# Kernel tuning notes

Measured on AMD Instinct MI355X. Metric: run time of the kernel, lower is better.

The kernel has to match this reference:

```python
import jax, jax.numpy as jnp
import numpy as np

B, T, C = 128, 512, 512
EPS = 1e-5


def setup_inputs() -> dict:
    key = jax.random.key(0)
    ks = jax.random.split(key, 12)
    s_tri = 1.0 / np.sqrt(T)   # rough torch Linear init scale (per-row fan-in varies; fixed for simplicity)
    s_fc1 = 1.0 / np.sqrt(C)
    s_fc2 = 1.0 / np.sqrt(2 * C)
    return {
        "inputs": jax.random.normal(ks[0], (B, T, C), dtype=jnp.float32),
        "ln1_w": jnp.ones((T, C), jnp.float32),
        "ln1_b": jnp.zeros((T, C), jnp.float32),
        "ln2_w": jnp.ones((T, C), jnp.float32),
        "ln2_b": jnp.zeros((T, C), jnp.float32),
        # Row s of triu_W corresponds to nn.Linear(s+1, 1); entries j> s are masked in reference().
        "triu_W": jax.random.uniform(ks[1], (T, T), jnp.float32, -s_tri, s_tri),
        "triu_b": jax.random.uniform(ks[2], (T,), jnp.float32, -s_tri, s_tri),
        "fc1_W": jax.random.uniform(ks[3], (2 * C, C), jnp.float32, -s_fc1, s_fc1),
        "fc1_b": jax.random.uniform(ks[4], (2 * C,), jnp.float32, -s_fc1, s_fc1),
        "fc2_W": jax.random.uniform(ks[5], (C, 2 * C), jnp.float32, -s_fc2, s_fc2),
        "fc2_b": jax.random.uniform(ks[6], (C,), jnp.float32, -s_fc2, s_fc2),
    }


def _layernorm_2d(x, w, b):
    # torch nn.LayerNorm((T, C)): normalize jointly over the last TWO dims.
    mu = jnp.mean(x, axis=(-2, -1), keepdims=True)
    var = jnp.var(x, axis=(-2, -1), keepdims=True)
    return (x - mu) * jax.lax.rsqrt(var + EPS) * w + b


def reference(inputs, ln1_w, ln1_b, ln2_w, ln2_b, triu_W, triu_b, fc1_W, fc1_b, fc2_W, fc2_b):
    x = _layernorm_2d(inputs, ln1_w, ln1_b)                       # [B,T,C]
    # TriU time mixer on x.mT ([B,C,T]): out[..., s] = sum_{t<=s} W[s,t]*x[..., t] + b[s]
    Wm = jnp.tril(triu_W)                                          # causal mask
    xm = jnp.einsum('btc,st->bsc', x, Wm) + triu_b[None, :, None]  # [B,T,C] (already back-transposed)
    x2 = _layernorm_2d(xm + inputs, ln2_w, ln2_b)                  # [B,T,C]
    h = jax.nn.gelu(jnp.einsum('btc,hc->bth', x2, fc1_W) + fc1_b, approximate=False)
    y = jnp.einsum('bth,ch->btc', h, fc2_W) + fc2_b
    return x2 + y
```

## Files before the change

### kernel.cpp

```cpp
#include <hip/hip_runtime.h>
#include <cstdint>

typedef unsigned short u16;
typedef __attribute__((ext_vector_type(8))) short s16x8;
typedef __attribute__((ext_vector_type(4))) float f32x4;
typedef __attribute__((ext_vector_type(8))) unsigned short u16x8;
typedef __attribute__((ext_vector_type(4))) unsigned short u16x4;

#define B_ 128
#define T_ 512
#define C_ 512
#define TC 262144

static __device__ __forceinline__ float bf2f(u16 u) {
  union { unsigned int i; float f; } v; v.i = ((unsigned int)u) << 16; return v.f;
}
static __device__ __forceinline__ u16 f2bf(float f) {
  union { float fv; unsigned int i; } v; v.fv = f;
  unsigned int r = (v.i + 0x7FFFu + ((v.i >> 16) & 1u)) >> 16;
  return (u16)r;
}

static __device__ __forceinline__ float gelu_fast(float x) {
  float x2 = x * x;
  float arg = 1.5957691216057308f * x * fmaf(0.044715f, x2, 1.0f);
  return x / (1.0f + __expf(-arg));
}

#define GLD16(gp, lp) __builtin_amdgcn_global_load_lds( \
    (const __attribute__((address_space(1))) void*)(gp), \
    (__attribute__((address_space(3))) void*)(lp), 16, 0, 0)


__global__ __launch_bounds__(256)
void reduce_stats_kernel(const float* __restrict__ X, float2* __restrict__ partials) {
  const int b = blockIdx.y, blk = blockIdx.x, tid = threadIdx.x;
  const float* p = X + (size_t)b * TC + (size_t)blk * 2048 + (size_t)tid * 8;
  f32x4 v0 = *(const f32x4*)p;
  f32x4 v1 = *(const f32x4*)(p + 4);
  float s = 0.f, q = 0.f;
#pragma unroll
  for (int i = 0; i < 4; ++i) { s += v0[i] + v1[i]; q += v0[i] * v0[i] + v1[i] * v1[i]; }
  for (int o = 32; o; o >>= 1) { s += __shfl_down(s, o); q += __shfl_down(q, o); }
  __shared__ float ss[4], qq[4];
  if ((tid & 63) == 0) { ss[tid >> 6] = s; qq[tid >> 6] = q; }
  __syncthreads();
  if (tid == 0)
    partials[(size_t)b * 128 + blk] =
        make_float2(ss[0] + ss[1] + ss[2] + ss[3], qq[0] + qq[1] + qq[2] + qq[3]);
}

__global__ __launch_bounds__(128)
void finalize_stats_kernel(const float2* __restrict__ partials, float2* __restrict__ stats) {
  const int b = blockIdx.x, tid = threadIdx.x;
  float2 v = partials[(size_t)b * 128 + tid];
  float s = v.x, q = v.y;
  for (int o = 32; o; o >>= 1) { s += __shfl_down(s, o); q += __shfl_down(q, o); }
  __shared__ float ss[2], qq[2];
  if ((tid & 63) == 0) { ss[tid >> 6] = s; qq[tid >> 6] = q; }
  __syncthreads();
  if (tid == 0) {
    float sm = ss[0] + ss[1], sq = qq[0] + qq[1];
    float mean = sm * (1.f / (float)TC);
    float var = sq * (1.f / (float)TC) - mean * mean;
    stats[b] = make_float2(mean, rsqrtf(var + 1e-5f));
  }
}

__global__ __launch_bounds__(64)
void finalize_stats4_kernel(const float2* __restrict__ partials, float2* __restrict__ stats) {
  const int b = blockIdx.x, tid = threadIdx.x;
  float s = 0.f, q = 0.f;
  if (tid < 4) { float2 v = partials[(size_t)b * 4 + tid]; s = v.x; q = v.y; }
  for (int o = 2; o; o >>= 1) { s += __shfl_down(s, o); q += __shfl_down(q, o); }
  if (tid == 0) {
    float mean = s * (1.f / (float)TC);
    float var = q * (1.f / (float)TC) - mean * mean;
    stats[b] = make_float2(mean, rsqrtf(var + 1e-5f));
  }
}


__global__ __launch_bounds__(256)
void ln1_transpose_kernel(const float* __restrict__ X, const float* __restrict__ W,
                          const float* __restrict__ Bv, const float2* __restrict__ stats,
                          u16* __restrict__ xT) {
  const int b = blockIdx.z;
  const int t0 = blockIdx.y * 64, c0 = blockIdx.x * 64;
  const float2 st = stats[b];
  const float mu = st.x, rs = st.y;
  __shared__ u16 tile[64][72];
  const int tid = threadIdx.x;
  const int rr = tid >> 4;
  const int cc = (tid & 15) * 4;
#pragma unroll
  for (int i = 0; i < 4; ++i) {
    const int lt = i * 16 + rr;
    const size_t wi = (size_t)(t0 + lt) * C_ + c0 + cc;
    f32x4 x = *(const f32x4*)(X + (size_t)b * TC + wi);
    f32x4 w = *(const f32x4*)(W + wi);
    f32x4 bb = *(const f32x4*)(Bv + wi);
#pragma unroll
    for (int j = 0; j < 4; ++j)
      tile[lt][cc + j] = f2bf((x[j] - mu) * rs * w[j] + bb[j]);
  }
  __syncthreads();
  const int c = tid >> 2;
  const int tg = (tid & 3) * 16;
  u16 buf[16];
#pragma unroll
  for (int i = 0; i < 16; ++i) buf[i] = tile[tg + i][c];
  const size_t o = (size_t)b * TC + (size_t)(c0 + c) * T_ + t0 + tg;
  u16x8 o0, o1;
#pragma unroll
  for (int i = 0; i < 8; ++i) { o0[i] = buf[i]; o1[i] = buf[8 + i]; }
  *(u16x8*)(xT + o) = o0;
  *(u16x8*)(xT + o + 8) = o1;
}


__global__ __launch_bounds__(256)
void ln2_apply_kernel(const u16* __restrict__ S, const float* __restrict__ W,
                      const float* __restrict__ Bv, const float2* __restrict__ stats,
                      u16* __restrict__ x2) {
  const size_t i = ((size_t)blockIdx.x * 256 + threadIdx.x) * 8;
  const int b = (int)(i >> 18);
  const size_t r = i & (size_t)(TC - 1);
  const float2 st = stats[b];
  const float mu = st.x, rs = st.y;
  u16x8 sv = *(const u16x8*)(S + i);
  f32x4 w0 = *(const f32x4*)(W + r);
  f32x4 w1 = *(const f32x4*)(W + r + 4);
  f32x4 b0 = *(const f32x4*)(Bv + r);
  f32x4 b1 = *(const f32x4*)(Bv + r + 4);
  u16x8 o;
#pragma unroll
  for (int j = 0; j < 4; ++j) {
    o[j]     = f2bf((bf2f(sv[j])     - mu) * rs * w0[j] + b0[j]);
    o[4 + j] = f2bf((bf2f(sv[4 + j]) - mu) * rs * w1[j] + b1[j]);
  }
  *(u16x8*)(x2 + i) = o;
}


__global__ __launch_bounds__(256)
void cvt_bf16_kernel(const float* __restrict__ X, u16* __restrict__ Y) {
  const size_t i = ((size_t)blockIdx.x * 256 + threadIdx.x) * 4;
  f32x4 v = *(const f32x4*)(X + i);
  u16x4 o;
#pragma unroll
  for (int j = 0; j < 4; ++j) o[j] = f2bf(v[j]);
  *(u16x4*)(Y + i) = o;
}

__global__ __launch_bounds__(256)
void tril_bf16_kernel(const float* __restrict__ Wt, u16* __restrict__ Y) {
  const int i = blockIdx.x * 256 + threadIdx.x;
  const int s = i >> 9, t = i & 511;
  Y[i] = f2bf(t <= s ? Wt[i] : 0.f);
}


template <int MODE>
__global__ __launch_bounds__(512, 1)
void gemm_bt_kernel(const u16* __restrict__ A, const u16* __restrict__ Bm,
                    int K, int lda, int ldb,
                    void* __restrict__ Cp, int ldc,
                    const float* __restrict__ bias,
                    const void* __restrict__ res,
                    long long strideB, long long strideC,
                    float2* __restrict__ stat_part) {
  __shared__ u16 Asb[2 * 16384];
  __shared__ u16 Bsb[2 * 16384];
  __shared__ float rs_[8], rq_[8];
  const int tid = threadIdx.x;

  const int nwg = gridDim.x;
  const int orig = blockIdx.x;
  const int swz = (orig & 7) * (nwg >> 3) + (orig >> 3);
  int bx, by, bz;
  if (MODE == 0) { bz = swz >> 2; by = (swz >> 1) & 1; bx = swz & 1; }
  else if (MODE == 1) { bz = 0; by = swz >> 2; bx = swz & 3; }
  else { bz = 0; by = swz >> 1; bx = swz & 1; }

  const u16* Bp = Bm + (size_t)bz * (size_t)strideB;
  const int m0 = by * 256, n0 = bx * 256;
  int kTiles = K >> 6;
  if (MODE == 0) { const int need = (by + 1) * 4; if (need < kTiles) kTiles = need; }

  const int lane = tid & 63;
  const int wave = tid >> 6;
  const int wm = (wave >> 2) * 128;
  const int wn = (wave & 3) * 64;
  const int lr = lane & 15;
  const int kg = lane >> 4;

  f32x4 acc[8][4];
  const f32x4 zero = {0.f, 0.f, 0.f, 0.f};
#pragma unroll
  for (int m = 0; m < 8; ++m)
#pragma unroll
    for (int n = 0; n < 4; ++n) acc[m][n] = zero;

  auto STAGE_A = [&](int t) {
    const int k0 = t << 6;
    const int d = (t & 1) * 16384;
#pragma unroll
    for (int p = 0; p < 4; ++p) {
      const int q = p * 512 + tid;
      const int r = q >> 3;
      const int kcs = (q & 7) ^ (r & 7);
      GLD16(A + (size_t)(m0 + r) * lda + k0 + (kcs << 3), &Asb[d + q * 8]);
    }
  };
  auto STAGE_B = [&](int t) {
    const int k0 = t << 6;
    const int d = (t & 1) * 16384;
#pragma unroll
    for (int p = 0; p < 4; ++p) {
      const int q = p * 512 + tid;
      const int r = q >> 3;
      const int kcs = (q & 7) ^ (r & 7);
      GLD16(Bp + (size_t)(n0 + r) * ldb + k0 + (kcs << 3), &Bsb[d + q * 8]);
    }
  };

  STAGE_A(0); STAGE_B(0); STAGE_A(1);

  for (int kt = 0; kt < kTiles; ++kt) {
    const int d = (kt & 1) * 16384;

    if (kt + 1 < kTiles) asm volatile("s_waitcnt vmcnt(4)" ::: "memory");
    else                 asm volatile("s_waitcnt vmcnt(0)" ::: "memory");
    __builtin_amdgcn_s_barrier();
    asm volatile("" ::: "memory");

    s16x8 a0[8], a1[8], b0[4], b1[4];
#pragma unroll
    for (int m = 0; m < 8; ++m) {
      const int row = wm + m * 16 + lr;
      const u16* base = &Asb[d + row * 64];
      a0[m] = *(const s16x8*)(base + (((kg)     ^ (row & 7)) << 3));
      a1[m] = *(const s16x8*)(base + (((4 + kg) ^ (row & 7)) << 3));
    }
#pragma unroll
    for (int n = 0; n < 4; ++n) {
      const int row = wn + n * 16 + lr;
      b0[n] = *(const s16x8*)(&Bsb[d + row * 64] + (((kg) ^ (row & 7)) << 3));
    }
    if (kt + 1 < kTiles) STAGE_B(kt + 1);

    __builtin_amdgcn_s_setprio(1);
#pragma unroll
    for (int m = 0; m < 8; ++m)
#pragma unroll
      for (int n = 0; n < 4; ++n)
        acc[m][n] = __builtin_amdgcn_mfma_f32_16x16x32_bf16(a0[m], b0[n], acc[m][n], 0, 0, 0);
    __builtin_amdgcn_s_setprio(0);

#pragma unroll
    for (int n = 0; n < 4; ++n) {
      const int row = wn + n * 16 + lr;
      b1[n] = *(const s16x8*)(&Bsb[d + row * 64] + (((4 + kg) ^ (row & 7)) << 3));
    }
    asm volatile("s_waitcnt lgkmcnt(0)" ::: "memory");
    __builtin_amdgcn_s_barrier();
    asm volatile("" ::: "memory");
    if (kt + 2 < kTiles) STAGE_A(kt + 2);

    __builtin_amdgcn_s_setprio(1);
#pragma unroll
    for (int m = 0; m < 8; ++m)
#pragma unroll
      for (int n = 0; n < 4; ++n)
        acc[m][n] = __builtin_amdgcn_mfma_f32_16x16x32_bf16(a1[m], b1[n], acc[m][n], 0, 0, 0);
    __builtin_amdgcn_s_setprio(0);
  }

  if (MODE == 0) {
    u16* Cptr = (u16*)Cp + (size_t)bz * (size_t)strideC;
    const float* inp = (const float*)res + (size_t)bz * (size_t)strideC;
    float psum = 0.f, psq = 0.f;
#pragma unroll
    for (int m = 0; m < 8; ++m) {
      const int rb = m0 + wm + m * 16 + kg * 4;
#pragma unroll
      for (int n = 0; n < 4; ++n) {
        const int col = n0 + wn + n * 16 + lr;
#pragma unroll
        for (int j = 0; j < 4; ++j) {
          const size_t idx = (size_t)(rb + j) * ldc + col;
          float v = acc[m][n][j] + inp[idx] + bias[rb + j];
          psum += v; psq += v * v;
          Cptr[idx] = f2bf(v);
        }
      }
    }
    for (int o = 32; o; o >>= 1) { psum += __shfl_down(psum, o); psq += __shfl_down(psq, o); }
    if (lane == 0) { rs_[wave] = psum; rq_[wave] = psq; }
    __syncthreads();
    if (tid == 0) {
      float s = 0.f, q = 0.f;
#pragma unroll
      for (int w = 0; w < 8; ++w) { s += rs_[w]; q += rq_[w]; }
      stat_part[(size_t)bz * 4 + by * 2 + bx] = make_float2(s, q);
    }
  } else if (MODE == 1) {
    u16* Cptr = (u16*)Cp;
#pragma unroll
    for (int m = 0; m < 8; ++m) {
      const int rb = m0 + wm + m * 16 + kg * 4;
#pragma unroll
      for (int n = 0; n < 4; ++n) {
        const int col = n0 + wn + n * 16 + lr;
        const float bs = bias[col];
#pragma unroll
        for (int j = 0; j < 4; ++j) {
          float v = acc[m][n][j] + bs;
          Cptr[(size_t)(rb + j) * ldc + col] = f2bf(gelu_fast(v));
        }
      }
    }
  } else {
    float* Cptr = (float*)Cp;
    const u16* x2p = (const u16*)res;
#pragma unroll
    for (int m = 0; m < 8; ++m) {
      const int rb = m0 + wm + m * 16 + kg * 4;
#pragma unroll
      for (int n = 0; n < 4; ++n) {
        const int col = n0 + wn + n * 16 + lr;
        const float bs = bias[col];
#pragma unroll
        for (int j = 0; j < 4; ++j) {
          const size_t idx = (size_t)(rb + j) * ldc + col;
          Cptr[idx] = acc[m][n][j] + bs + bf2f(x2p[idx]);
        }
      }
    }
  }
}


extern "C" void kernel_launch(void* const* d_in, const int* in_sizes, int n_in,
                              void* d_out, int out_size, void* d_ws, size_t ws_size,
                              hipStream_t stream) {
  const float* inputs = (const float*)d_in[0];
  const float* ln1_w  = (const float*)d_in[1];
  const float* ln1_b  = (const float*)d_in[2];
  const float* ln2_w  = (const float*)d_in[3];
  const float* ln2_b  = (const float*)d_in[4];
  const float* triu_W = (const float*)d_in[5];
  const float* triu_b = (const float*)d_in[6];
  const float* fc1_W  = (const float*)d_in[7];
  const float* fc1_b  = (const float*)d_in[8];
  const float* fc2_W  = (const float*)d_in[9];
  const float* fc2_b  = (const float*)d_in[10];
  float* out = (float*)d_out;
  (void)in_sizes; (void)n_in; (void)out_size; (void)ws_size;

  char* ws = (char*)d_ws;
  size_t off = 0;
  auto carve = [&](size_t bytes) {
    char* p = ws + off;
    off += (bytes + 255) & ~(size_t)255;
    return p;
  };
  u16* s_bf = (u16*)carve((size_t)B_ * T_ * C_ * 2);
  u16* xT   = (u16*)carve((size_t)B_ * T_ * C_ * 2);
  u16* x2   = xT;
  u16* h    = (u16*)carve((size_t)B_ * T_ * 2 * C_ * 2);
  u16* wmb  = (u16*)carve((size_t)T_ * T_ * 2);
  u16* w1b  = (u16*)carve((size_t)2 * C_ * C_ * 2);
  u16* w2b  = (u16*)carve((size_t)C_ * 2 * C_ * 2);
  float2* partials  = (float2*)carve(128 * 128 * sizeof(float2));
  float2* partials2 = (float2*)carve(128 * 4 * sizeof(float2));
  float2* stats1 = (float2*)carve(128 * sizeof(float2));
  float2* stats2 = (float2*)carve(128 * sizeof(float2));

  reduce_stats_kernel<<<dim3(128, 128), 256, 0, stream>>>(inputs, partials);
  finalize_stats_kernel<<<128, 128, 0, stream>>>(partials, stats1);
  ln1_transpose_kernel<<<dim3(8, 8, 128), 256, 0, stream>>>(inputs, ln1_w, ln1_b, stats1, xT);
  tril_bf16_kernel<<<1024, 256, 0, stream>>>(triu_W, wmb);
  cvt_bf16_kernel<<<512, 256, 0, stream>>>(fc1_W, w1b);
  cvt_bf16_kernel<<<512, 256, 0, stream>>>(fc2_W, w2b);
  gemm_bt_kernel<0><<<512, 512, 0, stream>>>(
      wmb, xT, 512, 512, 512, s_bf, 512, triu_b, inputs, (long long)TC, (long long)TC, partials2);
  finalize_stats4_kernel<<<128, 64, 0, stream>>>(partials2, stats2);
  ln2_apply_kernel<<<16384, 256, 0, stream>>>(s_bf, ln2_w, ln2_b, stats2, x2);
  gemm_bt_kernel<1><<<1024, 512, 0, stream>>>(
      x2, w1b, 512, 512, 512, h, 1024, fc1_b, nullptr, 0, 0, nullptr);
  gemm_bt_kernel<2><<<512, 512, 0, stream>>>(
      h, w2b, 1024, 1024, 1024, out, 512, fc2_b, x2, 0, 0, nullptr);
}
```

Measured before the change: 373.3 us.

## Load GEMM weights directly from global into registers, triple-buffer activations

For the FC GEMM modes, the weight (B) operand is no longer staged through shared memory; each wave loads its B fragments straight from global memory into registers, and the A tile gets a third LDS buffer so two tiles can be in flight ahead. This drops B LDS writes and reads and one barrier per k-step, and frees LDS for the extra A stage. The cost is uncached-by-LDS global loads of weights that are duplicated across waves, and the register loads may stall the MFMA issue if L2 latency isn't hidden. The vmcnt(4) wait count also now has the register loads mixed into the counter, which could make the synchronisation fragile.

```diff
diff --git a/kernel.cpp b/kernel.cpp
--- a/kernel.cpp
+++ b/kernel.cpp
@@ -170,8 +170,9 @@
                     const void* __restrict__ res,
                     long long strideB, long long strideC,
                     float2* __restrict__ stat_part) {
-  __shared__ u16 Asb[2 * 16384];
-  __shared__ u16 Bsb[2 * 16384];
+  constexpr int ABUFS = (MODE == 0) ? 2 : 3;
+  __shared__ u16 Asb[ABUFS * 16384];
+  __shared__ u16 Bsb[(MODE == 0) ? 2 * 16384 : 16];
   __shared__ float rs_[8], rq_[8];
   const int tid = threadIdx.x;
 
@@ -202,9 +203,9 @@
 #pragma unroll
     for (int n = 0; n < 4; ++n) acc[m][n] = zero;
 
-  auto STAGE_A = [&](int t) {
+  auto STAGE_A = [&](int t, int buf) {
     const int k0 = t << 6;
-    const int d = (t & 1) * 16384;
+    const int d = buf * 16384;
 #pragma unroll
     for (int p = 0; p < 4; ++p) {
       const int q = p * 512 + tid;
@@ -225,56 +226,101 @@
     }
   };
 
-  STAGE_A(0); STAGE_B(0); STAGE_A(1);
-
-  for (int kt = 0; kt < kTiles; ++kt) {
-    const int d = (kt & 1) * 16384;
-
-    if (kt + 1 < kTiles) asm volatile("s_waitcnt vmcnt(4)" ::: "memory");
-    else                 asm volatile("s_waitcnt vmcnt(0)" ::: "memory");
-    __builtin_amdgcn_s_barrier();
-    asm volatile("" ::: "memory");
-
-    s16x8 a0[8], a1[8], b0[4], b1[4];
-#pragma unroll
-    for (int m = 0; m < 8; ++m) {
-      const int row = wm + m * 16 + lr;
-      const u16* base = &Asb[d + row * 64];
-      a0[m] = *(const s16x8*)(base + (((kg)     ^ (row & 7)) << 3));
-      a1[m] = *(const s16x8*)(base + (((4 + kg) ^ (row & 7)) << 3));
-    }
-#pragma unroll
-    for (int n = 0; n < 4; ++n) {
-      const int row = wn + n * 16 + lr;
-      b0[n] = *(const s16x8*)(&Bsb[d + row * 64] + (((kg) ^ (row & 7)) << 3));
-    }
-    if (kt + 1 < kTiles) STAGE_B(kt + 1);
-
-    __builtin_amdgcn_s_setprio(1);
-#pragma unroll
-    for (int m = 0; m < 8; ++m)
-#pragma unroll
-      for (int n = 0; n < 4; ++n)
-        acc[m][n] = __builtin_amdgcn_mfma_f32_16x16x32_bf16(a0[m], b0[n], acc[m][n], 0, 0, 0);
-    __builtin_amdgcn_s_setprio(0);
-
-#pragma unroll
-    for (int n = 0; n < 4; ++n) {
-      const int row = wn + n * 16 + lr;
-      b1[n] = *(const s16x8*)(&Bsb[d + row * 64] + (((4 + kg) ^ (row & 7)) << 3));
-    }
-    asm volatile("s_waitcnt lgkmcnt(0)" ::: "memory");
-    __builtin_amdgcn_s_barrier();
-    asm volatile("" ::: "memory");
-    if (kt + 2 < kTiles) STAGE_A(kt + 2);
-
-    __builtin_amdgcn_s_setprio(1);
-#pragma unroll
-    for (int m = 0; m < 8; ++m)
-#pragma unroll
-      for (int n = 0; n < 4; ++n)
-        acc[m][n] = __builtin_amdgcn_mfma_f32_16x16x32_bf16(a1[m], b1[n], acc[m][n], 0, 0, 0);
-    __builtin_amdgcn_s_setprio(0);
+  if (MODE == 0) {
+    STAGE_A(0, 0); STAGE_B(0); STAGE_A(1, 1);
+    for (int kt = 0; kt < kTiles; ++kt) {
+      const int d = (kt & 1) * 16384;
+      if (kt + 1 < kTiles) asm volatile("s_waitcnt vmcnt(4)" ::: "memory");
+      else                 asm volatile("s_waitcnt vmcnt(0)" ::: "memory");
+      __builtin_amdgcn_s_barrier();
+      asm volatile("" ::: "memory");
+
+      s16x8 a0[8], a1[8], b0[4], b1[4];
+#pragma unroll
+      for (int m = 0; m < 8; ++m) {
+        const int row = wm + m * 16 + lr;
+        const u16* base = &Asb[d + row * 64];
+        a0[m] = *(const s16x8*)(base + (((kg)     ^ (row & 7)) << 3));
+        a1[m] = *(const s16x8*)(base + (((4 + kg) ^ (row & 7)) << 3));
+      }
+#pragma unroll
+      for (int n = 0; n < 4; ++n) {
+        const int row = wn + n * 16 + lr;
+        b0[n] = *(const s16x8*)(&Bsb[d + row * 64] + (((kg) ^ (row & 7)) << 3));
+      }
+      if (kt + 1 < kTiles) STAGE_B(kt + 1);
+
+      __builtin_amdgcn_s_setprio(1);
+#pragma unroll
+      for (int m = 0; m < 8; ++m)
+#pragma unroll
+        for (int n = 0; n < 4; ++n)
+          acc[m][n] = __builtin_amdgcn_mfma_f32_16x16x32_bf16(a0[m], b0[n], acc[m][n], 0, 0, 0);
+      __builtin_amdgcn_s_setprio(0);
+
+#pragma unroll
+      for (int n = 0; n < 4; ++n) {
+        const int row = wn + n * 16 + lr;
+        b1[n] = *(const s16x8*)(&Bsb[d + row * 64] + (((4 + kg) ^ (row & 7)) << 3));
+      }
+      asm volatile("s_waitcnt lgkmcnt(0)" ::: "memory");
+      __builtin_amdgcn_s_barrier();
+      asm volatile("" ::: "memory");
+      if (kt + 2 < kTiles) STAGE_A(kt + 2, kt & 1);
+
+      __builtin_amdgcn_s_setprio(1);
+#pragma unroll
+      for (int m = 0; m < 8; ++m)
+#pragma unroll
+        for (int n = 0; n < 4; ++n)
+          acc[m][n] = __builtin_amdgcn_mfma_f32_16x16x32_bf16(a1[m], b1[n], acc[m][n], 0, 0, 0);
+      __builtin_amdgcn_s_setprio(0);
+    }
+  } else {
+    int rb0 = 0, rb1 = 1, rb2 = 2;
+    STAGE_A(0, 0); STAGE_A(1, 1);
+    for (int kt = 0; kt < kTiles; ++kt) {
+      const int k0 = kt << 6;
+      if (kt + 1 < kTiles) asm volatile("s_waitcnt vmcnt(4)" ::: "memory");
+      else                 asm volatile("s_waitcnt vmcnt(0)" ::: "memory");
+      __builtin_amdgcn_s_barrier();
+      asm volatile("" ::: "memory");
+
+      s16x8 w0[4], w1[4];
+#pragma unroll
+      for (int n = 0; n < 4; ++n) {
+        const u16* wrow = Bp + (size_t)(n0 + wn + n * 16 + lr) * ldb + k0 + (kg << 3);
+        w0[n] = *(const s16x8*)wrow;
+        w1[n] = *(const s16x8*)(wrow + 32);
+      }
+      asm volatile("" ::: "memory");
+      if (kt + 2 < kTiles) STAGE_A(kt + 2, rb2);
+
+      const int d = rb0 * 16384;
+      s16x8 a0[8], a1[8];
+#pragma unroll
+      for (int m = 0; m < 8; ++m) {
+        const int row = wm + m * 16 + lr;
+        const u16* base = &Asb[d + row * 64];
+        a0[m] = *(const s16x8*)(base + (((kg)     ^ (row & 7)) << 3));
+        a1[m] = *(const s16x8*)(base + (((4 + kg) ^ (row & 7)) << 3));
+      }
+
+      __builtin_amdgcn_s_setprio(1);
+#pragma unroll
+      for (int m = 0; m < 8; ++m)
+#pragma unroll
+        for (int n = 0; n < 4; ++n)
+          acc[m][n] = __builtin_amdgcn_mfma_f32_16x16x32_bf16(a0[m], w0[n], acc[m][n], 0, 0, 0);
+#pragma unroll
+      for (int m = 0; m < 8; ++m)
+#pragma unroll
+        for (int n = 0; n < 4; ++n)
+          acc[m][n] = __builtin_amdgcn_mfma_f32_16x16x32_bf16(a1[m], w1[n], acc[m][n], 0, 0, 0);
+      __builtin_amdgcn_s_setprio(0);
+
+      const int t = rb0; rb0 = rb1; rb1 = rb2; rb2 = t;
+    }
   }
 
   if (MODE == 0) {
```

After: 457.9 us. +22.7%, slower.

## Use FP8 for FC2 GEMM and bf16 copy of inputs for LN1 and residual

Applied to the files above, without the earlier changes.

The GELU output h and the fc2 weights are now stored as FP8 e4m3, and the FC2 GEMM runs on fp8 MFMA with half-size LDS tiles, allowing two blocks per CU. The stats reduction also writes a bf16 copy of the inputs, which the LN1 transpose and the triu GEMM residual read instead of fp32. This halves memory traffic for h and the input re-reads and doubles MFMA throughput for FC2. In exchange it loses precision, since FP8 h with GELU outputs and the bf16 residual may push the error past tolerance, and it adds an extra write of the inputs.

```diff
diff --git a/kernel.cpp b/kernel.cpp
--- a/kernel.cpp
+++ b/kernel.cpp
@@ -1,11 +1,14 @@
 #include <hip/hip_runtime.h>
+#include <hip/hip_fp8.h>
 #include <cstdint>
 
 typedef unsigned short u16;
+typedef unsigned char u8;
 typedef __attribute__((ext_vector_type(8))) short s16x8;
 typedef __attribute__((ext_vector_type(4))) float f32x4;
 typedef __attribute__((ext_vector_type(8))) unsigned short u16x8;
 typedef __attribute__((ext_vector_type(4))) unsigned short u16x4;
+typedef __attribute__((ext_vector_type(4))) unsigned char u8x4;
 
 #define B_ 128
 #define T_ 512
@@ -20,6 +23,10 @@
   unsigned int r = (v.i + 0x7FFFu + ((v.i >> 16) & 1u)) >> 16;
   return (u16)r;
 }
+static __device__ __forceinline__ u8 f2fp8(float f) {
+  __hip_fp8_e4m3 v(f);
+  return *(u8*)&v;
+}
 
 static __device__ __forceinline__ float gelu_fast(float x) {
   float x2 = x * x;
@@ -33,14 +40,21 @@
 
 
 __global__ __launch_bounds__(256)
-void reduce_stats_kernel(const float* __restrict__ X, float2* __restrict__ partials) {
+void reduce_stats_kernel(const float* __restrict__ X, float2* __restrict__ partials,
+                         u16* __restrict__ Xb) {
   const int b = blockIdx.y, blk = blockIdx.x, tid = threadIdx.x;
-  const float* p = X + (size_t)b * TC + (size_t)blk * 2048 + (size_t)tid * 8;
+  const size_t gi = (size_t)b * TC + (size_t)blk * 2048 + (size_t)tid * 8;
+  const float* p = X + gi;
   f32x4 v0 = *(const f32x4*)p;
   f32x4 v1 = *(const f32x4*)(p + 4);
   float s = 0.f, q = 0.f;
-#pragma unroll
-  for (int i = 0; i < 4; ++i) { s += v0[i] + v1[i]; q += v0[i] * v0[i] + v1[i] * v1[i]; }
+  u16x8 ob;
+#pragma unroll
+  for (int i = 0; i < 4; ++i) {
+    s += v0[i] + v1[i]; q += v0[i] * v0[i] + v1[i] * v1[i];
+    ob[i] = f2bf(v0[i]); ob[4 + i] = f2bf(v1[i]);
+  }
+  *(u16x8*)(Xb + gi) = ob;
   for (int o = 32; o; o >>= 1) { s += __shfl_down(s, o); q += __shfl_down(q, o); }
   __shared__ float ss[4], qq[4];
   if ((tid & 63) == 0) { ss[tid >> 6] = s; qq[tid >> 6] = q; }
@@ -82,7 +96,7 @@
 
 
 __global__ __launch_bounds__(256)
-void ln1_transpose_kernel(const float* __restrict__ X, const float* __restrict__ W,
+void ln1_transpose_kernel(const u16* __restrict__ Xb, const float* __restrict__ W,
                           const float* __restrict__ Bv, const float2* __restrict__ stats,
                           u16* __restrict__ xT) {
   const int b = blockIdx.z;
@@ -97,12 +111,12 @@
   for (int i = 0; i < 4; ++i) {
     const int lt = i * 16 + rr;
     const size_t wi = (size_t)(t0 + lt) * C_ + c0 + cc;
-    f32x4 x = *(const f32x4*)(X + (size_t)b * TC + wi);
+    u16x4 xa = *(const u16x4*)(Xb + (size_t)b * TC + wi);
     f32x4 w = *(const f32x4*)(W + wi);
     f32x4 bb = *(const f32x4*)(Bv + wi);
 #pragma unroll
     for (int j = 0; j < 4; ++j)
-      tile[lt][cc + j] = f2bf((x[j] - mu) * rs * w[j] + bb[j]);
+      tile[lt][cc + j] = f2bf((bf2f(xa[j]) - mu) * rs * w[j] + bb[j]);
   }
   __syncthreads();
   const int c = tid >> 2;
@@ -154,6 +168,16 @@
 }
 
 __global__ __launch_bounds__(256)
+void cvt_fp8_kernel(const float* __restrict__ X, u8* __restrict__ Y) {
+  const size_t i = ((size_t)blockIdx.x * 256 + threadIdx.x) * 4;
+  f32x4 v = *(const f32x4*)(X + i);
+  u8x4 o;
+#pragma unroll
+  for (int j = 0; j < 4; ++j) o[j] = f2fp8(v[j]);
+  *(u8x4*)(Y + i) = o;
+}
+
+__global__ __launch_bounds__(256)
 void tril_bf16_kernel(const float* __restrict__ Wt, u16* __restrict__ Y) {
   const int i = blockIdx.x * 256 + threadIdx.x;
   const int s = i >> 9, t = i & 511;
@@ -162,7 +186,7 @@
 
 
 template <int MODE>
-__global__ __launch_bounds__(512, 1)
+__global__ __launch_bounds__(512, (MODE == 2) ? 2 : 1)
 void gemm_bt_kernel(const u16* __restrict__ A, const u16* __restrict__ Bm,
                     int K, int lda, int ldb,
                     void* __restrict__ Cp, int ldc,
@@ -170,8 +194,9 @@
                     const void* __restrict__ res,
                     long long strideB, long long strideC,
                     float2* __restrict__ stat_part) {
-  __shared__ u16 Asb[2 * 16384];
-  __shared__ u16 Bsb[2 * 16384];
+  constexpr int TILE_U16 = (MODE == 2) ? 8192 : 16384;
+  __shared__ u16 Asb[2 * TILE_U16];
+  __shared__ u16 Bsb[2 * TILE_U16];
   __shared__ float rs_[8], rq_[8];
   const int tid = threadIdx.x;
 
@@ -224,62 +249,142 @@
       GLD16(Bp + (size_t)(n0 + r) * ldb + k0 + (kcs << 3), &Bsb[d + q * 8]);
     }
   };
-
-  STAGE_A(0); STAGE_B(0); STAGE_A(1);
-
-  for (int kt = 0; kt < kTiles; ++kt) {
-    const int d = (kt & 1) * 16384;
-
-    if (kt + 1 < kTiles) asm volatile("s_waitcnt vmcnt(4)" ::: "memory");
-    else                 asm volatile("s_waitcnt vmcnt(0)" ::: "memory");
-    __builtin_amdgcn_s_barrier();
-    asm volatile("" ::: "memory");
-
-    s16x8 a0[8], a1[8], b0[4], b1[4];
-#pragma unroll
-    for (int m = 0; m < 8; ++m) {
-      const int row = wm + m * 16 + lr;
-      const u16* base = &Asb[d + row * 64];
-      a0[m] = *(const s16x8*)(base + (((kg)     ^ (row & 7)) << 3));
-      a1[m] = *(const s16x8*)(base + (((4 + kg) ^ (row & 7)) << 3));
-    }
-#pragma unroll
-    for (int n = 0; n < 4; ++n) {
-      const int row = wn + n * 16 + lr;
-      b0[n] = *(const s16x8*)(&Bsb[d + row * 64] + (((kg) ^ (row & 7)) << 3));
-    }
-    if (kt + 1 < kTiles) STAGE_B(kt + 1);
-
-    __builtin_amdgcn_s_setprio(1);
-#pragma unroll
-    for (int m = 0; m < 8; ++m)
-#pragma unroll
-      for (int n = 0; n < 4; ++n)
-        acc[m][n] = __builtin_amdgcn_mfma_f32_16x16x32_bf16(a0[m], b0[n], acc[m][n], 0, 0, 0);
-    __builtin_amdgcn_s_setprio(0);
-
-#pragma unroll
-    for (int n = 0; n < 4; ++n) {
-      const int row = wn + n * 16 + lr;
-      b1[n] = *(const s16x8*)(&Bsb[d + row * 64] + (((4 + kg) ^ (row & 7)) << 3));
-    }
-    asm volatile("s_waitcnt lgkmcnt(0)" ::: "memory");
-    __builtin_amdgcn_s_barrier();
-    asm volatile("" ::: "memory");
-    if (kt + 2 < kTiles) STAGE_A(kt + 2);
-
-    __builtin_amdgcn_s_setprio(1);
-#pragma unroll
-    for (int m = 0; m < 8; ++m)
-#pragma unroll
-      for (int n = 0; n < 4; ++n)
-        acc[m][n] = __builtin_amdgcn_mfma_f32_16x16x32_bf16(a1[m], b1[n], acc[m][n], 0, 0, 0);
-    __builtin_amdgcn_s_setprio(0);
+  auto STAGE_A8 = [&](int t) {
+    const int k0 = t << 6;
+    u8* lds = (u8*)Asb + (t & 1) * 16384;
+    const u8* src = (const u8*)A;
+#pragma unroll
+    for (int p = 0; p < 2; ++p) {
+      const int q = p * 512 + tid;
+      const int r = q >> 2;
+      const int c16 = (q & 3) ^ ((r >> 2) & 3);
+      GLD16(src + (size_t)(m0 + r) * lda + k0 + c16 * 16, lds + q * 16);
+    }
+  };
+  auto STAGE_B8 = [&](int t) {
+    const int k0 = t << 6;
+    u8* lds = (u8*)Bsb + (t & 1) * 16384;
+    const u8* src = (const u8*)Bp;
+#pragma unroll
+    for (int p = 0; p < 2; ++p) {
+      const int q = p * 512 + tid;
+      const int r = q >> 2;
+      const int c16 = (q & 3) ^ ((r >> 2) & 3);
+      GLD16(src + (size_t)(n0 + r) * ldb + k0 + c16 * 16, lds + q * 16);
+    }
+  };
+
+  if (MODE != 2) {
+    STAGE_A(0); STAGE_B(0); STAGE_A(1);
+    for (int kt = 0; kt < kTiles; ++kt) {
+      const int d = (kt & 1) * 16384;
+      if (kt + 1 < kTiles) asm volatile("s_waitcnt vmcnt(4)" ::: "memory");
+      else                 asm volatile("s_waitcnt vmcnt(0)" ::: "memory");
+      __builtin_amdgcn_s_barrier();
+      asm volatile("" ::: "memory");
+
+      s16x8 a0[8], a1[8], b0[4], b1[4];
+#pragma unroll
+      for (int m = 0; m < 8; ++m) {
+        const int row = wm + m * 16 + lr;
+        const u16* base = &Asb[d + row * 64];
+        a0[m] = *(const s16x8*)(base + (((kg)     ^ (row & 7)) << 3));
+        a1[m] = *(const s16x8*)(base + (((4 + kg) ^ (row & 7)) << 3));
+      }
+#pragma unroll
+      for (int n = 0; n < 4; ++n) {
+        const int row = wn + n * 16 + lr;
+        b0[n] = *(const s16x8*)(&Bsb[d + row * 64] + (((kg) ^ (row & 7)) << 3));
+      }
+      if (kt + 1 < kTiles) STAGE_B(kt + 1);
+
+      __builtin_amdgcn_s_setprio(1);
+#pragma unroll
+      for (int m = 0; m < 8; ++m)
+#pragma unroll
+        for (int n = 0; n < 4; ++n)
+          acc[m][n] = __builtin_amdgcn_mfma_f32_16x16x32_bf16(a0[m], b0[n], acc[m][n], 0, 0, 0);
+      __builtin_amdgcn_s_setprio(0);
+
+#pragma unroll
+      for (int n = 0; n < 4; ++n) {
+        const int row = wn + n * 16 + lr;
+        b1[n] = *(const s16x8*)(&Bsb[d + row * 64] + (((4 + kg) ^ (row & 7)) << 3));
+      }
+      asm volatile("s_waitcnt lgkmcnt(0)" ::: "memory");
+      __builtin_amdgcn_s_barrier();
+      asm volatile("" ::: "memory");
+      if (kt + 2 < kTiles) STAGE_A(kt + 2);
+
+      __builtin_amdgcn_s_setprio(1);
+#pragma unroll
+      for (int m = 0; m < 8; ++m)
+#pragma unroll
+        for (int n = 0; n < 4; ++n)
+          acc[m][n] = __builtin_amdgcn_mfma_f32_16x16x32_bf16(a1[m], b1[n], acc[m][n], 0, 0, 0);
+      __builtin_amdgcn_s_setprio(0);
+    }
+  } else {
+    STAGE_A8(0); STAGE_B8(0); STAGE_A8(1);
+    for (int kt = 0; kt < kTiles; ++kt) {
+      const u8* Ad = (const u8*)Asb + (kt & 1) * 16384;
+      const u8* Bd = (const u8*)Bsb + (kt & 1) * 16384;
+      if (kt + 1 < kTiles) asm volatile("s_waitcnt vmcnt(2)" ::: "memory");
+      else                 asm volatile("s_waitcnt vmcnt(0)" ::: "memory");
+      __builtin_amdgcn_s_barrier();
+      asm volatile("" ::: "memory");
+
+      long a0[8], a1[8], b0[4], b1[4];
+      const int sub = (kg & 1) * 8;
+      const int hi = kg >> 1;
+#pragma unroll
+      for (int m = 0; m < 8; ++m) {
+        const int row = wm + m * 16 + lr;
+        const u8* base = Ad + row * 64;
+        const int sw = (row >> 2) & 3;
+        a0[m] = *(const long*)(base + ((hi)     ^ sw) * 16 + sub);
+        a1[m] = *(const long*)(base + ((2 + hi) ^ sw) * 16 + sub);
+      }
+#pragma unroll
+      for (int n = 0; n < 4; ++n) {
+        const int row = wn + n * 16 + lr;
+        const int sw = (row >> 2) & 3;
+        b0[n] = *(const long*)(Bd + row * 64 + ((hi) ^ sw) * 16 + sub);
+      }
+      if (kt + 1 < kTiles) STAGE_B8(kt + 1);
+
+      __builtin_amdgcn_s_setprio(1);
+#pragma unroll
+      for (int m = 0; m < 8; ++m)
+#pragma unroll
+        for (int n = 0; n < 4; ++n)
+          acc[m][n] = __builtin_amdgcn_mfma_f32_16x16x32_fp8_fp8(a0[m], b0[n], acc[m][n], 0, 0, 0);
+      __builtin_amdgcn_s_setprio(0);
+
+#pragma unroll
+      for (int n = 0; n < 4; ++n) {
+        const int row = wn + n * 16 + lr;
+        const int sw = (row >> 2) & 3;
+        b1[n] = *(const long*)(Bd + row * 64 + ((2 + hi) ^ sw) * 16 + sub);
+      }
+      asm volatile("s_waitcnt lgkmcnt(0)" ::: "memory");
+      __builtin_amdgcn_s_barrier();
+      asm volatile("" ::: "memory");
+      if (kt + 2 < kTiles) STAGE_A8(kt + 2);
+
+      __builtin_amdgcn_s_setprio(1);
+#pragma unroll
+      for (int m = 0; m < 8; ++m)
+#pragma unroll
+        for (int n = 0; n < 4; ++n)
+          acc[m][n] = __builtin_amdgcn_mfma_f32_16x16x32_fp8_fp8(a1[m], b1[n], acc[m][n], 0, 0, 0);
+      __builtin_amdgcn_s_setprio(0);
+    }
   }
 
   if (MODE == 0) {
     u16* Cptr = (u16*)Cp + (size_t)bz * (size_t)strideC;
-    const float* inp = (const float*)res + (size_t)bz * (size_t)strideC;
+    const u16* inp = (const u16*)res + (size_t)bz * (size_t)strideC;
     float psum = 0.f, psq = 0.f;
 #pragma unroll
     for (int m = 0; m < 8; ++m) {
@@ -290,7 +395,7 @@
 #pragma unroll
         for (int j = 0; j < 4; ++j) {
           const size_t idx = (size_t)(rb + j) * ldc + col;
-          float v = acc[m][n][j] + inp[idx] + bias[rb + j];
+          float v = acc[m][n][j] + bf2f(inp[idx]) + bias[rb + j];
           psum += v; psq += v * v;
           Cptr[idx] = f2bf(v);
         }
@@ -306,7 +411,7 @@
       stat_part[(size_t)bz * 4 + by * 2 + bx] = make_float2(s, q);
     }
   } else if (MODE == 1) {
-    u16* Cptr = (u16*)Cp;
+    u8* Cptr = (u8*)Cp;
 #pragma unroll
     for (int m = 0; m < 8; ++m) {
       const int rb = m0 + wm + m * 16 + kg * 4;
@@ -317,7 +422,7 @@
 #pragma unroll
         for (int j = 0; j < 4; ++j) {
           float v = acc[m][n][j] + bs;
-          Cptr[(size_t)(rb + j) * ldc + col] = f2bf(gelu_fast(v));
+          Cptr[(size_t)(rb + j) * ldc + col] = f2fp8(gelu_fast(v));
         }
       }
     }
@@ -369,27 +474,28 @@
   u16* s_bf = (u16*)carve((size_t)B_ * T_ * C_ * 2);
   u16* xT   = (u16*)carve((size_t)B_ * T_ * C_ * 2);
   u16* x2   = xT;
-  u16* h    = (u16*)carve((size_t)B_ * T_ * 2 * C_ * 2);
+  u16* inb  = (u16*)carve((size_t)B_ * T_ * C_ * 2);
+  u8*  h    = (u8*)carve((size_t)B_ * T_ * 2 * C_);
   u16* wmb  = (u16*)carve((size_t)T_ * T_ * 2);
   u16* w1b  = (u16*)carve((size_t)2 * C_ * C_ * 2);
-  u16* w2b  = (u16*)carve((size_t)C_ * 2 * C_ * 2);
+  u8*  w2f8 = (u8*)carve((size_t)C_ * 2 * C_);
   float2* partials  = (float2*)carve(128 * 128 * sizeof(float2));
   float2* partials2 = (float2*)carve(128 * 4 * sizeof(float2));
   float2* stats1 = (float2*)carve(128 * sizeof(float2));
   float2* stats2 = (float2*)carve(128 * sizeof(float2));
 
-  reduce_stats_kernel<<<dim3(128, 128), 256, 0, stream>>>(inputs, partials);
+  reduce_stats_kernel<<<dim3(128, 128), 256, 0, stream>>>(inputs, partials, inb);
   finalize_stats_kernel<<<128, 128, 0, stream>>>(partials, stats1);
-  ln1_transpose_kernel<<<dim3(8, 8, 128), 256, 0, stream>>>(inputs, ln1_w, ln1_b, stats1, xT);
+  ln1_transpose_kernel<<<dim3(8, 8, 128), 256, 0, stream>>>(inb, ln1_w, ln1_b, stats1, xT);
   tril_bf16_kernel<<<1024, 256, 0, stream>>>(triu_W, wmb);
   cvt_bf16_kernel<<<512, 256, 0, stream>>>(fc1_W, w1b);
-  cvt_bf16_kernel<<<512, 256, 0, stream>>>(fc2_W, w2b);
+  cvt_fp8_kernel<<<512, 256, 0, stream>>>(fc2_W, w2f8);
   gemm_bt_kernel<0><<<512, 512, 0, stream>>>(
-      wmb, xT, 512, 512, 512, s_bf, 512, triu_b, inputs, (long long)TC, (long long)TC, partials2);
+      wmb, xT, 512, 512, 512, s_bf, 512, triu_b, inb, (long long)TC, (long long)TC, partials2);
   finalize_stats4_kernel<<<128, 64, 0, stream>>>(partials2, stats2);
   ln2_apply_kernel<<<16384, 256, 0, stream>>>(s_bf, ln2_w, ln2_b, stats2, x2);
   gemm_bt_kernel<1><<<1024, 512, 0, stream>>>(
       x2, w1b, 512, 512, 512, h, 1024, fc1_b, nullptr, 0, 0, nullptr);
   gemm_bt_kernel<2><<<512, 512, 0, stream>>>(
-      h, w2b, 1024, 1024, 1024, out, 512, fc2_b, x2, 0, 0, nullptr);
-}
+      (const u16*)h, (const u16*)w2f8, 1024, 1024, 1024, out, 512, fc2_b, x2, 0, 0, nullptr);
+}
```

Result: faster. 356.0 us (-4.6%).
